# Performance work log

Hardware: AMD Instinct MI355X
Metric: run time of the kernel (lower is better)

The kernel has to match this reference:

```python
import jax, jax.numpy as jnp
import numpy as np

Z_DIM = 3
H = 128
N_BLOCKS = 4
N = 30000
E = 180000
T = 2


def _mlp2(x, W1, b1, W2, b2):
    return jnp.maximum(x @ W1 + b1, 0.0) @ W2 + b2


def _stats(x, eps=1e-8):
    # batch mean/std as accumulated by the running-stat Normalizer (buffers -> no grad)
    m = x.mean(0)
    v = jnp.maximum((x * x).mean(0) - m * m, 0.0)
    s = jnp.maximum(jnp.sqrt(v), eps)
    return jax.lax.stop_gradient(m), jax.lax.stop_gradient(s)


def setup_inputs() -> dict:
    key = jax.random.key(0)
    ks = jax.random.split(key, 32)

    def w(k, shape, fan_in):
        return jax.random.normal(k, shape, jnp.float32) / np.sqrt(fan_in).astype(np.float32)

    inp = {}
    inp["z"] = jax.random.normal(ks[0], (T, N, Z_DIM), jnp.float32)
    inp["z_target"] = jax.random.normal(ks[1], (N, Z_DIM), jnp.float32)
    inp["pos"] = jax.random.uniform(ks[2], (N, 2), jnp.float32)
    # encoder node MLP: z_dim -> H -> H
    inp["enc_node_W1"] = w(ks[3], (Z_DIM, H), Z_DIM)
    inp["enc_node_b1"] = jnp.zeros((H,), jnp.float32)
    inp["enc_node_W2"] = w(ks[4], (H, H), H)
    inp["enc_node_b2"] = jnp.zeros((H,), jnp.float32)
    # encoder edge MLP: edge_dim(3) -> H -> H
    inp["enc_edge_W1"] = w(ks[5], (3, H), 3)
    inp["enc_edge_b1"] = jnp.zeros((H,), jnp.float32)
    inp["enc_edge_W2"] = w(ks[6], (H, H), H)
    inp["enc_edge_b2"] = jnp.zeros((H,), jnp.float32)
    # decoder MLP: H -> H -> z_dim
    inp["dec_W1"] = w(ks[7], (H, H), H)
    inp["dec_b1"] = jnp.zeros((H,), jnp.float32)
    inp["dec_W2"] = w(ks[8], (H, Z_DIM), H)
    inp["dec_b2"] = jnp.zeros((Z_DIM,), jnp.float32)
    # GraphNetBlocks, stacked over n_blocks
    inp["blk_edge_W1"] = w(ks[9], (N_BLOCKS, 3 * H, H), 3 * H)
    inp["blk_edge_b1"] = jnp.zeros((N_BLOCKS, H), jnp.float32)
    inp["blk_edge_W2"] = w(ks[10], (N_BLOCKS, H, H), H)
    inp["blk_edge_b2"] = jnp.zeros((N_BLOCKS, H), jnp.float32)
    inp["blk_node_W1"] = w(ks[11], (N_BLOCKS, 2 * H, H), 2 * H)
    inp["blk_node_b1"] = jnp.zeros((N_BLOCKS, H), jnp.float32)
    inp["blk_node_W2"] = w(ks[12], (N_BLOCKS, H, H), H)
    inp["blk_node_b2"] = jnp.zeros((N_BLOCKS, H), jnp.float32)
    # bidirectional mesh edges (triangles_to_edges output)
    inp["senders"] = jax.random.randint(ks[13], (E,), 0, N, jnp.int64)
    inp["receivers"] = jax.random.randint(ks[14], (E,), 0, N, jnp.int64)
    return inp


def reference(z, z_target, pos,
              enc_node_W1, enc_node_b1, enc_node_W2, enc_node_b2,
              enc_edge_W1, enc_edge_b1, enc_edge_W2, enc_edge_b2,
              dec_W1, dec_b1, dec_W2, dec_b2,
              blk_edge_W1, blk_edge_b1, blk_edge_W2, blk_edge_b2,
              blk_node_W1, blk_node_b1, blk_node_W2, blk_node_b2,
              senders, receivers):
    zl = z[-1]                                   # [N, z_dim]
    n_nodes = zl.shape[0]

    # --- build_graph ---
    rel = pos[senders] - pos[receivers]          # [E, 2]
    ef_raw = jnp.concatenate([rel, jnp.linalg.norm(rel, axis=1, keepdims=True)], axis=1)  # [E, 3]
    em, es = _stats(ef_raw)
    ef = _mlp2((ef_raw - em) / es, enc_edge_W1, enc_edge_b1, enc_edge_W2, enc_edge_b2)    # [E, H]
    nm, ns = _stats(zl)
    nf = _mlp2((zl - nm) / ns, enc_node_W1, enc_node_b1, enc_node_W2, enc_node_b2)        # [N, H]

    # --- message passing blocks ---
    def block(carry, p):
        nf, ef = carry
        eW1, eb1, eW2, eb2, nW1, nb1, nW2, nb2 = p
        e_in = jnp.concatenate([ef, nf[senders], nf[receivers]], axis=1)   # [E, 3H]
        ef = _mlp2(e_in, eW1, eb1, eW2, eb2) + ef
        agg = jax.ops.segment_sum(ef, receivers, num_segments=n_nodes)    # [N, H]
        n_in = jnp.concatenate([nf, agg], axis=1)                          # [N, 2H]
        nf = _mlp2(n_in, nW1, nb1, nW2, nb2) + nf
        return (nf, ef), None

    (nf, ef), _ = jax.lax.scan(block, (nf, ef),
                               (blk_edge_W1, blk_edge_b1, blk_edge_W2, blk_edge_b2,
                                blk_node_W1, blk_node_b1, blk_node_W2, blk_node_b2))

    # --- decode + loss ---
    output = _mlp2(nf, dec_W1, dec_b1, dec_W2, dec_b2)                     # [N, z_dim]
    target = z_target - zl
    om, os = _stats(target)
    target_normalized = (target - om) / os
    loss = jnp.mean((target_normalized - output) ** 2)

    z_update = jax.lax.stop_gradient(output) * os + om                     # Normalizer.inverse(detach)
    z_pred = zl + z_update
    rmse = jnp.mean(jnp.sqrt(jnp.mean((z_pred - z_target) ** 2, axis=0)))
    return z_pred, loss, rmse
```

## Files before the change

### kernel.cpp

```cpp
#include <hip/hip_runtime.h>
#include <hip/hip_bf16.h>
#include <math.h>

#define HDIM 128
#define TPB 256

typedef __attribute__((ext_vector_type(8))) short bf16x8;
typedef __attribute__((ext_vector_type(4))) float f32x4;

static inline int ceil_div(int a, int b){ return (a + b - 1) / b; }

__device__ __forceinline__ float wave_sum(float v){
#pragma unroll
  for (int o = 32; o > 0; o >>= 1) v += __shfl_down(v, o, 64);
  return v;
}
__device__ __forceinline__ int wave_sum_i(int v){
#pragma unroll
  for (int o = 32; o > 0; o >>= 1) v += __shfl_down(v, o, 64);
  return v;
}

__device__ __forceinline__ short f2bf(float f){
  __hip_bfloat16 h = __float2bfloat16(f);
  return *reinterpret_cast<short*>(&h);
}
__device__ __forceinline__ float bfb2f(short s){
  unsigned int u = ((unsigned int)(unsigned short)s) << 16;
  return __builtin_bit_cast(float, u);
}

__device__ __forceinline__ void gl_lds16(const short* g, short* l){
  __builtin_amdgcn_global_load_lds(
      (const __attribute__((address_space(1))) void*)g,
      (__attribute__((address_space(3))) void*)l, 16, 0, 0);
}

__global__ void prep_a(const int* __restrict__ rcv, int* __restrict__ deg, int E, int neb,
                       const float* __restrict__ zl, const float* __restrict__ zt,
                       float* __restrict__ npart, int N, int nnb,
                       const float* __restrict__ encEW2,
                       const float* __restrict__ encNW2,
                       const float* __restrict__ decW1,
                       const float* __restrict__ beW1,
                       const float* __restrict__ beW2,
                       const float* __restrict__ bnW1,
                       const float* __restrict__ bnW2,
                       __hip_bfloat16* __restrict__ wp){
  __shared__ float red[4][12];
  const int bx = blockIdx.x, tid = threadIdx.x;
  if (bx < neb){
    int e = bx * 256 + tid;
    if (e < E) atomicAdd(&deg[rcv[e]], 1);
    return;
  }
  if (bx < neb + nnb){
    int b = bx - neb;
    int w = tid >> 6, l = tid & 63;
    int n = b * 256 + tid;
    float s[12];
#pragma unroll
    for (int i = 0; i < 12; i++) s[i] = 0.f;
    if (n < N){
#pragma unroll
      for (int d = 0; d < 3; d++){
        float z = zl[3*n+d];
        float t = zt[3*n+d] - z;
        s[d]   = z;  s[3+d] = z*z;
        s[6+d] = t;  s[9+d] = t*t;
      }
    }
#pragma unroll
    for (int i = 0; i < 12; i++) s[i] = wave_sum(s[i]);
    if (l == 0)
#pragma unroll
      for (int i = 0; i < 12; i++) red[w][i] = s[i];
    __syncthreads();
    if (tid < 12)
      npart[(size_t)b * 12 + tid] =
        red[0][tid] + red[1][tid] + red[2][tid] + red[3][tid];
    return;
  }
  int pid = bx - neb - nnb;
  int y = pid / 192;
  int x = pid - y * 192;
  const float* src; __hip_bfloat16* dst; int K;
  if (y == 0){ src = encEW2; dst = wp;          K = 128; }
  else if (y == 1){ src = encNW2; dst = wp + 16384; K = 128; }
  else if (y == 2){ src = decW1;  dst = wp + 32768; K = 128; }
  else {
    int b = (y - 3) >> 2, j = (y - 3) & 3;
    __hip_bfloat16* base = wp + 49152 + b * 114688;
    if (j == 0){ src = beW1 + b*49152; dst = base;          K = 384; }
    else if (j == 1){ src = beW2 + b*16384; dst = base + 49152; K = 128; }
    else if (j == 2){ src = bnW1 + b*32768; dst = base + 65536; K = 256; }
    else { src = bnW2 + b*16384; dst = base + 98304; K = 128; }
  }
  int id = x * 256 + tid;
  if (id >= 128 * K) return;
  int c = id >> 12;
  int r = id & 4095;
  int t = r >> 9;
  int l = (r >> 3) & 63;
  int j = r & 7;
  int k = c * 32 + ((l >> 4) << 3) + j;
  int n = t * 16 + (l & 15);
  dst[id] = __float2bfloat16(src[k * 128 + n]);
}

__global__ void scan_pass1(const int* __restrict__ deg, int* __restrict__ bsum, int N){
  __shared__ int red[4];
  int tid = threadIdx.x;
  int base = blockIdx.x * 1024;
  int s = 0;
  for (int i = tid; i < 1024; i += 256){
    int idx = base + i;
    if (idx < N) s += deg[idx];
  }
  s = wave_sum_i(s);
  if ((tid & 63) == 0) red[tid >> 6] = s;
  __syncthreads();
  if (tid == 0) bsum[blockIdx.x] = red[0] + red[1] + red[2] + red[3];
}

__global__ void scan_pass3(const int* __restrict__ deg, const int* __restrict__ bsum,
                           int nsb, int* __restrict__ row_start,
                           int* __restrict__ cursor, int N, int E){
  __shared__ int tsum[256];
  __shared__ int base_s;
  int tid = threadIdx.x;
  if (tid == 0){
    int acc = 0;
    for (int b = 0; b < (int)blockIdx.x; b++) acc += bsum[b];
    base_s = acc;
    if (blockIdx.x == 0) row_start[N] = E;
  }
  int base = blockIdx.x * 1024;
  int i0 = base + tid * 4;
  int v[4];
  int s = 0;
#pragma unroll
  for (int k = 0; k < 4; k++){
    int idx = i0 + k;
    v[k] = (idx < N) ? deg[idx] : 0;
    s += v[k];
  }
  tsum[tid] = s;
  __syncthreads();
  for (int off = 1; off < 256; off <<= 1){
    int val = (tid >= off) ? tsum[tid - off] : 0;
    __syncthreads();
    tsum[tid] += val;
    __syncthreads();
  }
  int excl = (tid == 0) ? 0 : tsum[tid - 1];
  int b = base_s + excl;
#pragma unroll
  for (int k = 0; k < 4; k++){
    int idx = i0 + k;
    if (idx < N){
      row_start[idx] = b;
      cursor[idx]    = b;
      b += v[k];
    }
  }
}

__global__ void edge_prep(const float* __restrict__ pos,
                          const int* __restrict__ snd,
                          const int* __restrict__ rcv,
                          int* __restrict__ cursor,
                          int* __restrict__ psnd,
                          int* __restrict__ prcv,
                          float* __restrict__ ef_raw,
                          float* __restrict__ epart, int E){
  __shared__ float red[4][6];
  int tid = threadIdx.x, w = tid >> 6, l = tid & 63;
  int e = blockIdx.x * blockDim.x + tid;
  float s[6] = {0.f,0.f,0.f,0.f,0.f,0.f};
  if (e < E){
    int si = snd[e], ri = rcv[e];
    int p = atomicAdd(&cursor[ri], 1);
    psnd[p] = si;
    prcv[p] = ri;
    float rx = pos[2*si]   - pos[2*ri];
    float ry = pos[2*si+1] - pos[2*ri+1];
    float nm = sqrtf(rx*rx + ry*ry);
    ef_raw[3*p]   = rx;
    ef_raw[3*p+1] = ry;
    ef_raw[3*p+2] = nm;
    s[0] = rx; s[1] = ry; s[2] = nm;
    s[3] = rx*rx; s[4] = ry*ry; s[5] = nm*nm;
  }
#pragma unroll
  for (int k = 0; k < 6; k++) s[k] = wave_sum(s[k]);
  if (l == 0)
#pragma unroll
    for (int k = 0; k < 6; k++) red[w][k] = s[k];
  __syncthreads();
  if (tid < 6)
    epart[(size_t)blockIdx.x * 6 + tid] =
      red[0][tid] + red[1][tid] + red[2][tid] + red[3][tid];
}

__global__ void reduce_finalize(const float* __restrict__ ep, int ne,
                                const float* __restrict__ np_, int nn,
                                float* __restrict__ fin, int E, int N){
  __shared__ float red[4];
  __shared__ float raw[18];
  int tid = threadIdx.x, w = tid >> 6, l = tid & 63;
  for (int j = 0; j < 6; j++){
    float s = 0.f;
    for (int b = tid; b < ne; b += 256) s += ep[(size_t)b * 6 + j];
    s = wave_sum(s);
    if (l == 0) red[w] = s;
    __syncthreads();
    if (tid == 0) raw[j] = red[0] + red[1] + red[2] + red[3];
    __syncthreads();
  }
  for (int j = 0; j < 12; j++){
    float s = 0.f;
    for (int b = tid; b < nn; b += 256) s += np_[(size_t)b * 12 + j];
    s = wave_sum(s);
    if (l == 0) red[w] = s;
    __syncthreads();
    if (tid == 0) raw[6 + j] = red[0] + red[1] + red[2] + red[3];
    __syncthreads();
  }
  if (tid == 0){
#pragma unroll
    for (int d = 0; d < 3; d++){
      float cE = (float)E, cN = (float)N;
      float m, v;
      m = raw[0+d] / cE; v = fmaxf(raw[3+d]/cE - m*m, 0.f);
      fin[0+d] = m;  fin[3+d]  = fmaxf(sqrtf(v), 1e-8f);
      m = raw[6+d] / cN; v = fmaxf(raw[9+d]/cN - m*m, 0.f);
      fin[6+d] = m;  fin[9+d]  = fmaxf(sqrtf(v), 1e-8f);
      m = raw[12+d] / cN; v = fmaxf(raw[15+d]/cN - m*m, 0.f);
      fin[12+d] = m; fin[15+d] = fmaxf(sqrtf(v), 1e-8f);
    }
  }
}

__launch_bounds__(256)
__global__ void encoder_both(const float* __restrict__ eraw,
                             const float* __restrict__ zl,
                             const float* __restrict__ fin,
                             const float* __restrict__ eW1, const float* __restrict__ eb1,
                             const float* __restrict__ nW1, const float* __restrict__ nb1,
                             const __hip_bfloat16* __restrict__ wp,
                             const float* __restrict__ eb2, const float* __restrict__ nb2,
                             __hip_bfloat16* __restrict__ efo, __hip_bfloat16* __restrict__ nfo,
                             int E, int N, int EB){
  __shared__ __align__(16) short bsh[16384];
  const int tid = threadIdx.x, w = tid >> 6, l = tid & 63, m = l & 15, q = l >> 4;
  const bool ise = ((int)blockIdx.x < EB);
  const float* raw = ise ? eraw : zl;
  const float* mptr = fin + (ise ? 0 : 6);
  const float* sptr = fin + (ise ? 3 : 9);
  const float* W1 = ise ? eW1 : nW1;
  const float* b1 = ise ? eb1 : nb1;
  const float* b2 = ise ? eb2 : nb2;
  const short* wsrc = (const short*)wp + (ise ? 0 : 16384);
  __hip_bfloat16* out = ise ? efo : nfo;
  const int rows = ise ? E : N;
  const int bx = ise ? (int)blockIdx.x : (int)blockIdx.x - EB;
#pragma unroll
  for (int i = 0; i < 8; i++){
    int inst = w * 8 + i;
    gl_lds16(wsrc + inst * 512 + l * 8, &bsh[inst * 512]);
  }
  float s0 = mptr[0], s1 = mptr[1], s2 = mptr[2];
  float d0 = sptr[0], d1 = sptr[1], d2 = sptr[2];
  const int row0 = bx * 64 + w * 16;
  const int ra = min(row0 + m, rows - 1);
  float x0 = (raw[3*ra]   - s0) / d0;
  float x1 = (raw[3*ra+1] - s1) / d1;
  float x2 = (raw[3*ra+2] - s2) / d2;
  bf16x8 afr[4];
#pragma unroll
  for (int c = 0; c < 4; c++){
    int nb = c * 32 + q * 8;
#pragma unroll
    for (int j = 0; j < 8; j++){
      float h = b1[nb+j] + x0 * W1[nb+j] + x1 * W1[128+nb+j] + x2 * W1[256+nb+j];
      afr[c][j] = f2bf(fmaxf(h, 0.f));
    }
  }
  f32x4 acc[8];
#pragma unroll
  for (int t = 0; t < 8; t++) acc[t] = (f32x4){0.f,0.f,0.f,0.f};
  __syncthreads();
#pragma unroll
  for (int c = 0; c < 4; c++){
#pragma unroll
    for (int t = 0; t < 8; t++){
      bf16x8 b = *(const bf16x8*)&bsh[(c*8 + t)*512 + l*8];
      acc[t] = __builtin_amdgcn_mfma_f32_16x16x32_bf16(afr[c], b, acc[t], 0, 0, 0);
    }
  }
  const int row_d = row0 + q * 4;
#pragma unroll
  for (int t = 0; t < 8; t++){
    int col = t * 16 + m;
    float bb = b2[col];
#pragma unroll
    for (int r = 0; r < 4; r++){
      int e = row_d + r;
      if (e < rows) out[(size_t)e * HDIM + col] = __float2bfloat16(acc[t][r] + bb);
    }
  }
}

__launch_bounds__(256)
__global__ void msg_pre(const __hip_bfloat16* __restrict__ nf,
                        const __hip_bfloat16* __restrict__ eWf,
                        __hip_bfloat16* __restrict__ u, int N){
  __shared__ __align__(16) short wsh[16384];
  const int tid = threadIdx.x, w = tid >> 6, l = tid & 63, m = l & 15, q = l >> 4;
  const short* wsrc = (const short*)eWf + 4 * 4096;
#pragma unroll
  for (int i = 0; i < 8; i++){
    int f = w * 8 + i;
    gl_lds16(wsrc + f * 512 + l * 8, &wsh[f * 512]);
  }
  const int row0 = blockIdx.x * 64 + w * 16;
  const int ra = min(row0 + m, N - 1);
  const short* pa = (const short*)nf + (size_t)ra * HDIM + q * 8;
  bf16x8 afr[4];
#pragma unroll
  for (int c = 0; c < 4; c++) afr[c] = *(const bf16x8*)(pa + c * 32);
  f32x4 acc[8];
#pragma unroll
  for (int t = 0; t < 8; t++) acc[t] = (f32x4){0.f,0.f,0.f,0.f};
  __syncthreads();
#pragma unroll
  for (int c = 0; c < 4; c++)
#pragma unroll
    for (int t = 0; t < 8; t++){
      bf16x8 b = *(const bf16x8*)&wsh[(c*8 + t)*512 + l*8];
      acc[t] = __builtin_amdgcn_mfma_f32_16x16x32_bf16(afr[c], b, acc[t], 0, 0, 0);
    }
  const int row_d = row0 + q * 4;
#pragma unroll
  for (int t = 0; t < 8; t++){
    int col = t * 16 + m;
#pragma unroll
    for (int r = 0; r < 4; r++){
      int n = row_d + r;
      if (n < N) u[(size_t)n * 256 + col] = __float2bfloat16(acc[t][r]);
    }
  }
  __syncthreads();
#pragma unroll
  for (int i = 0; i < 8; i++){
    int f = w * 8 + i;
    gl_lds16(wsrc + 16384 + f * 512 + l * 8, &wsh[f * 512]);
  }
#pragma unroll
  for (int t = 0; t < 8; t++) acc[t] = (f32x4){0.f,0.f,0.f,0.f};
  __syncthreads();
#pragma unroll
  for (int c = 0; c < 4; c++)
#pragma unroll
    for (int t = 0; t < 8; t++){
      bf16x8 b = *(const bf16x8*)&wsh[(c*8 + t)*512 + l*8];
      acc[t] = __builtin_amdgcn_mfma_f32_16x16x32_bf16(afr[c], b, acc[t], 0, 0, 0);
    }
#pragma unroll
  for (int t = 0; t < 8; t++){
    int col = 128 + t * 16 + m;
#pragma unroll
    for (int r = 0; r < 4; r++){
      int n = row_d + r;
      if (n < N) u[(size_t)n * 256 + col] = __float2bfloat16(acc[t][r]);
    }
  }
}

__launch_bounds__(512, 6)
__global__ void edge_block(const int* __restrict__ psnd,
                           const int* __restrict__ prcv,
                           const __hip_bfloat16* __restrict__ u,
                           __hip_bfloat16* __restrict__ ef,
                           const __hip_bfloat16* __restrict__ Wfrag,
                           const float* __restrict__ b1,
                           const float* __restrict__ b2,
                           int E){
  __shared__ __align__(16) short bsh[8192];
  __shared__ __align__(16) short hsh[8][16][136];
  const int tid = threadIdx.x, w = tid >> 6, l = tid & 63, m = l & 15, q = l >> 4;
  const short* wsrc = (const short*)Wfrag;
  const int row0 = blockIdx.x * 128 + w * 16;
  const int grow = min(row0 + (l >> 2), E - 1);
  const int us_row = psnd[grow], ur_row = prcv[grow];
  gl_lds16(wsrc + (w*2)  *512 + l*8, &bsh[(w*2)  *512]);
  gl_lds16(wsrc + (w*2+1)*512 + l*8, &bsh[(w*2+1)*512]);
  const int ra = min(row0 + m, E - 1);
  const short* pe = (const short*)ef + (size_t)ra * HDIM + q * 8;
  bf16x8 afr[4];
#pragma unroll
  for (int c = 0; c < 4; c++) afr[c] = *(const bf16x8*)(pe + c * 32);
  {
    const short* pus = (const short*)u + (size_t)us_row * 256 + (l & 3) * 32;
    const short* pur = (const short*)u + (size_t)ur_row * 256 + 128 + (l & 3) * 32;
    short* hdst = &hsh[w][l >> 2][(l & 3) * 32];
#pragma unroll
    for (int k = 0; k < 4; k++){
      bf16x8 a = *(const bf16x8*)(pus + k * 8);
      bf16x8 b = *(const bf16x8*)(pur + k * 8);
      bf16x8 s;
#pragma unroll
      for (int j = 0; j < 8; j++) s[j] = f2bf(bfb2f(a[j]) + bfb2f(b[j]));
      *(bf16x8*)(hdst + k * 8) = s;
    }
  }
  f32x4 acc[8];
#pragma unroll
  for (int t = 0; t < 8; t++) acc[t] = (f32x4){0.f,0.f,0.f,0.f};
  __syncthreads();
#pragma unroll
  for (int cc = 0; cc < 2; cc++)
#pragma unroll
    for (int t = 0; t < 8; t++){
      bf16x8 b = *(const bf16x8*)&bsh[(cc*8 + t)*512 + l*8];
      acc[t] = __builtin_amdgcn_mfma_f32_16x16x32_bf16(afr[cc], b, acc[t], 0, 0, 0);
    }
  __syncthreads();
  gl_lds16(wsrc + 8192 + (w*2)  *512 + l*8, &bsh[(w*2)  *512]);
  gl_lds16(wsrc + 8192 + (w*2+1)*512 + l*8, &bsh[(w*2+1)*512]);
  __syncthreads();
#pragma unroll
  for (int cc = 0; cc < 2; cc++)
#pragma unroll
    for (int t = 0; t < 8; t++){
      bf16x8 b = *(const bf16x8*)&bsh[(cc*8 + t)*512 + l*8];
      acc[t] = __builtin_amdgcn_mfma_f32_16x16x32_bf16(afr[2+cc], b, acc[t], 0, 0, 0);
    }
  __syncthreads();
  gl_lds16(wsrc + 49152 + (w*2)  *512 + l*8, &bsh[(w*2)  *512]);
  gl_lds16(wsrc + 49152 + (w*2+1)*512 + l*8, &bsh[(w*2+1)*512]);
#pragma unroll
  for (int t = 0; t < 8; t++){
    float bb = b1[t * 16 + m];
#pragma unroll
    for (int r = 0; r < 4; r++){
      float uval = bfb2f(hsh[w][q*4 + r][t*16 + m]);
      hsh[w][q*4 + r][t*16 + m] = f2bf(fmaxf(acc[t][r] + uval + bb, 0.f));
    }
  }
  __syncthreads();
  bf16x8 ah[4];
  const short* ph = &hsh[w][m][0] + q * 8;
#pragma unroll
  for (int c = 0; c < 4; c++) ah[c] = *(const bf16x8*)(ph + c * 32);
#pragma unroll
  for (int t = 0; t < 8; t++) acc[t] = (f32x4){0.f,0.f,0.f,0.f};
#pragma unroll
  for (int cc = 0; cc < 2; cc++)
#pragma unroll
    for (int t = 0; t < 8; t++){
      bf16x8 b = *(const bf16x8*)&bsh[(cc*8 + t)*512 + l*8];
      acc[t] = __builtin_amdgcn_mfma_f32_16x16x32_bf16(ah[cc], b, acc[t], 0, 0, 0);
    }
  __syncthreads();
  gl_lds16(wsrc + 57344 + (w*2)  *512 + l*8, &bsh[(w*2)  *512]);
  gl_lds16(wsrc + 57344 + (w*2+1)*512 + l*8, &bsh[(w*2+1)*512]);
  const int orow = row0 + (l >> 2);
  const int orc = min(orow, E - 1);
  const short* pold = (const short*)ef + (size_t)orc * HDIM + (l & 3) * 32;
  bf16x8 vold[4];
#pragma unroll
  for (int k = 0; k < 4; k++) vold[k] = *(const bf16x8*)(pold + k * 8);
  __syncthreads();
#pragma unroll
  for (int cc = 0; cc < 2; cc++)
#pragma unroll
    for (int t = 0; t < 8; t++){
      bf16x8 b = *(const bf16x8*)&bsh[(cc*8 + t)*512 + l*8];
      acc[t] = __builtin_amdgcn_mfma_f32_16x16x32_bf16(ah[2+cc], b, acc[t], 0, 0, 0);
    }
#pragma unroll
  for (int t = 0; t < 8; t++){
    float bb = b2[t * 16 + m];
#pragma unroll
    for (int r = 0; r < 4; r++)
      hsh[w][q*4 + r][t*16 + m] = f2bf(acc[t][r] + bb);
  }
  if (orow < E){
    const short* src = &hsh[w][l >> 2][(l & 3) * 32];
    short* dst = (short*)ef + (size_t)orow * HDIM + (l & 3) * 32;
#pragma unroll
    for (int k = 0; k < 4; k++){
      bf16x8 vnew = *(const bf16x8*)(src + k * 8);
      bf16x8 vr;
#pragma unroll
      for (int j = 0; j < 8; j++) vr[j] = f2bf(bfb2f(vnew[j]) + bfb2f(vold[k][j]));
      *(bf16x8*)(dst + k * 8) = vr;
    }
  }
}

#define NB_COMPUTE_CHUNK(c) do {                                               \
  const short* bb_ = &bsh[(((c) >> 1) & 1) * 8192 + ((c) & 1) * 4096];         \
  _Pragma("unroll")                                                            \
  for (int t = 0; t < 8; t++){                                                 \
    bf16x8 b = *(const bf16x8*)(bb_ + t * 512 + l * 8);                        \
    acc[t] = __builtin_amdgcn_mfma_f32_16x16x32_bf16(afr[c], b, acc[t], 0, 0, 0); \
  }                                                                            \
} while(0)

__launch_bounds__(256)
__global__ void node_block(const int* __restrict__ row_start,
                           const __hip_bfloat16* __restrict__ ef,
                           __hip_bfloat16* __restrict__ nf,
                           const __hip_bfloat16* __restrict__ Wfrag,
                           const float* __restrict__ b1,
                           const float* __restrict__ b2,
                           int N){
  __shared__ __align__(16) short bsh[16384];
  __shared__ __align__(16) short hsh[4][16][136];
  const int tid = threadIdx.x, w = tid >> 6, l = tid & 63, m = l & 15, q = l >> 4;
  const short* wsrc = (const short*)Wfrag;
  auto stage_pair = [&](int p){
    const short* s = wsrc + p * 8192;
    short* d = &bsh[(p & 1) * 8192];
#pragma unroll
    for (int i = 0; i < 4; i++)
      gl_lds16(s + (i*4 + w)*512 + l*8, d + (i*4 + w)*512);
  };
  stage_pair(0); stage_pair(1);

  const int row0 = blockIdx.x * 64 + w * 16;
  const int ra = min(row0 + m, N - 1);
  const short* pn = (const short*)nf + (size_t)ra * HDIM + q * 8;
  bf16x8 afr[8];
#pragma unroll
  for (int c = 0; c < 4; c++) afr[c] = *(const bf16x8*)(pn + c * 32);

  float sum[4][8];
#pragma unroll
  for (int c = 0; c < 4; c++)
#pragma unroll
    for (int j = 0; j < 8; j++) sum[c][j] = 0.f;
  int s0 = row_start[ra], s1 = row_start[ra + 1];
  for (int it = s0; it < s1; it++){
    const short* pf = (const short*)ef + (size_t)it * HDIM + q * 8;
#pragma unroll
    for (int c = 0; c < 4; c++){
      bf16x8 v = *(const bf16x8*)(pf + c * 32);
#pragma unroll
      for (int j = 0; j < 8; j++) sum[c][j] += bfb2f(v[j]);
    }
  }
#pragma unroll
  for (int c = 0; c < 4; c++)
#pragma unroll
    for (int j = 0; j < 8; j++) afr[4 + c][j] = f2bf(sum[c][j]);

  f32x4 acc[8];
#pragma unroll
  for (int t = 0; t < 8; t++) acc[t] = (f32x4){0.f,0.f,0.f,0.f};
  __syncthreads();
  NB_COMPUTE_CHUNK(0);
  NB_COMPUTE_CHUNK(1);
  __syncthreads();
  stage_pair(2);
  NB_COMPUTE_CHUNK(2);
  NB_COMPUTE_CHUNK(3);
  __syncthreads();
  stage_pair(3);
  NB_COMPUTE_CHUNK(4);
  NB_COMPUTE_CHUNK(5);
  __syncthreads();
  NB_COMPUTE_CHUNK(6);
  NB_COMPUTE_CHUNK(7);
  __syncthreads();
  {
    const short* s = wsrc + 32768;
#pragma unroll
    for (int i = 0; i < 8; i++)
      gl_lds16(s + (i*4 + w)*512 + l*8, &bsh[(i*4 + w)*512]);
  }
#pragma unroll
  for (int t = 0; t < 8; t++){
    float bb = b1[t * 16 + m];
#pragma unroll
    for (int r = 0; r < 4; r++)
      hsh[w][q*4 + r][t*16 + m] = f2bf(fmaxf(acc[t][r] + bb, 0.f));
  }
  __syncthreads();
  const short* ph = &hsh[w][m][0] + q * 8;
#pragma unroll
  for (int t = 0; t < 8; t++) acc[t] = (f32x4){0.f,0.f,0.f,0.f};
#pragma unroll
  for (int c = 0; c < 4; c++){
    bf16x8 a = *(const bf16x8*)(ph + c * 32);
#pragma unroll
    for (int t = 0; t < 8; t++){
      bf16x8 b = *(const bf16x8*)&bsh[(c*8 + t)*512 + l*8];
      acc[t] = __builtin_amdgcn_mfma_f32_16x16x32_bf16(a, b, acc[t], 0, 0, 0);
    }
  }
#pragma unroll
  for (int t = 0; t < 8; t++){
    float bb = b2[t * 16 + m];
#pragma unroll
    for (int r = 0; r < 4; r++)
      hsh[w][q*4 + r][t*16 + m] = f2bf(acc[t][r] + bb);
  }
  const int orow = row0 + (l >> 2);
  if (orow < N){
    const short* pold = (const short*)nf + (size_t)orow * HDIM + (l & 3) * 32;
    const short* src = &hsh[w][l >> 2][(l & 3) * 32];
    short* dst = (short*)nf + (size_t)orow * HDIM + (l & 3) * 32;
#pragma unroll
    for (int k = 0; k < 4; k++){
      bf16x8 vnew = *(const bf16x8*)(src + k * 8);
      bf16x8 vo   = *(const bf16x8*)(pold + k * 8);
      bf16x8 vr;
#pragma unroll
      for (int j = 0; j < 8; j++) vr[j] = f2bf(bfb2f(vnew[j]) + bfb2f(vo[j]));
      *(bf16x8*)(dst + k * 8) = vr;
    }
  }
}

__launch_bounds__(256)
__global__ void dec_fused(const __hip_bfloat16* __restrict__ A,
                          const __hip_bfloat16* __restrict__ Wf,
                          const float* __restrict__ b1,
                          const float* __restrict__ W2,
                          const float* __restrict__ b2,
                          const float* __restrict__ zl,
                          const float* __restrict__ z_target,
                          const float* __restrict__ fin,
                          float* __restrict__ d_out,
                          float* __restrict__ lred,
                          unsigned int* __restrict__ cnt,
                          int N){
  __shared__ __align__(16) short bsh[16384];
  __shared__ float Wl[HDIM * 3];
  __shared__ float red[4][4];
  const int tid = threadIdx.x, w = tid >> 6, l = tid & 63, m = l & 15, q = l >> 4;
  const short* wsrc = (const short*)Wf;
#pragma unroll
  for (int i = 0; i < 8; i++){
    int inst = w * 8 + i;
    gl_lds16(wsrc + inst * 512 + l * 8, &bsh[inst * 512]);
  }
  for (int i = tid; i < HDIM * 3; i += 256) Wl[i] = W2[i];
  const int row0 = blockIdx.x * 64 + w * 16;
  const int ra = min(row0 + m, N - 1);
  const short* pa = (const short*)A + (size_t)ra * HDIM + q * 8;
  bf16x8 afr[4];
#pragma unroll
  for (int c = 0; c < 4; c++) afr[c] = *(const bf16x8*)(pa + c * 32);
  f32x4 acc[8];
#pragma unroll
  for (int t = 0; t < 8; t++) acc[t] = (f32x4){0.f,0.f,0.f,0.f};
  __syncthreads();
#pragma unroll
  for (int c = 0; c < 4; c++){
#pragma unroll
    for (int t = 0; t < 8; t++){
      bf16x8 b = *(const bf16x8*)&bsh[(c*8 + t)*512 + l*8];
      acc[t] = __builtin_amdgcn_mfma_f32_16x16x32_bf16(afr[c], b, acc[t], 0, 0, 0);
    }
  }
  float p0[4] = {0,0,0,0}, p1[4] = {0,0,0,0}, p2[4] = {0,0,0,0};
#pragma unroll
  for (int t = 0; t < 8; t++){
    int col = t * 16 + m;
    float bb = b1[col];
    float w0 = Wl[col*3], w1 = Wl[col*3+1], w2 = Wl[col*3+2];
#pragma unroll
    for (int r = 0; r < 4; r++){
      float h = fmaxf(acc[t][r] + bb, 0.f);
      p0[r] += h * w0; p1[r] += h * w1; p2[r] += h * w2;
    }
  }
#pragma unroll
  for (int r = 0; r < 4; r++){
#pragma unroll
    for (int o = 1; o < 16; o <<= 1){
      p0[r] += __shfl_xor(p0[r], o, 64);
      p1[r] += __shfl_xor(p1[r], o, 64);
      p2[r] += __shfl_xor(p2[r], o, 64);
    }
  }
  float s[4] = {0.f,0.f,0.f,0.f};
  if (m == 0){
#pragma unroll
    for (int r = 0; r < 4; r++){
      int n = row0 + q * 4 + r;
      if (n < N){
        float pd[3] = {p0[r], p1[r], p2[r]};
#pragma unroll
        for (int d = 0; d < 3; d++){
          float o   = pd[d] + b2[d];
          float om = fin[12 + d], os = fin[15 + d];
          float zld = zl[3*n + d];
          float zt  = z_target[3*n + d];
          float tn  = ((zt - zld) - om) / os;
          float diff = tn - o;
          s[0] += diff * diff;
          float zp = zld + o * os + om;
          d_out[3*n + d] = zp;
          float e = zp - zt;
          s[1 + d] += e * e;
        }
      }
    }
  }
#pragma unroll
  for (int k = 0; k < 4; k++) s[k] = wave_sum(s[k]);
  if (l == 0)
#pragma unroll
    for (int k = 0; k < 4; k++) red[w][k] = s[k];
  __syncthreads();
  if (tid < 4)
    atomicAdd(&lred[tid], red[0][tid] + red[1][tid] + red[2][tid] + red[3][tid]);
  __syncthreads();
  if (tid == 0){
    __threadfence();
    unsigned int t = atomicAdd(cnt, 1u);
    if (t == gridDim.x - 1){
      float vals[4];
#pragma unroll
      for (int k = 0; k < 4; k++) vals[k] = atomicAdd(&lred[k], 0.f);
      float cN = (float)N;
      float loss = vals[0] / (3.f * cN);
      float rmse = (sqrtf(vals[1]/cN) + sqrtf(vals[2]/cN) + sqrtf(vals[3]/cN)) / 3.f;
      d_out[(size_t)3 * N]     = loss;
      d_out[(size_t)3 * N + 1] = rmse;
    }
  }
}

extern "C" void kernel_launch(void* const* d_in, const int* in_sizes, int n_in,
                              void* d_out, int out_size, void* d_ws, size_t ws_size,
                              hipStream_t stream){
  const float* z           = (const float*)d_in[0];
  const float* z_target    = (const float*)d_in[1];
  const float* pos         = (const float*)d_in[2];
  const float* enc_node_W1 = (const float*)d_in[3];
  const float* enc_node_b1 = (const float*)d_in[4];
  const float* enc_node_W2 = (const float*)d_in[5];
  const float* enc_node_b2 = (const float*)d_in[6];
  const float* enc_edge_W1 = (const float*)d_in[7];
  const float* enc_edge_b1 = (const float*)d_in[8];
  const float* enc_edge_W2 = (const float*)d_in[9];
  const float* enc_edge_b2 = (const float*)d_in[10];
  const float* dec_W1      = (const float*)d_in[11];
  const float* dec_b1      = (const float*)d_in[12];
  const float* dec_W2      = (const float*)d_in[13];
  const float* dec_b2      = (const float*)d_in[14];
  const float* blk_edge_W1 = (const float*)d_in[15];
  const float* blk_edge_b1 = (const float*)d_in[16];
  const float* blk_edge_W2 = (const float*)d_in[17];
  const float* blk_edge_b2 = (const float*)d_in[18];
  const float* blk_node_W1 = (const float*)d_in[19];
  const float* blk_node_b1 = (const float*)d_in[20];
  const float* blk_node_W2 = (const float*)d_in[21];
  const float* blk_node_b2 = (const float*)d_in[22];
  const int*   senders     = (const int*)d_in[23];
  const int*   receivers   = (const int*)d_in[24];

  const int N = in_sizes[1] / 3;
  const int E = in_sizes[23];
  const float* zl = z + (size_t)N * 3;

  const int neb = ceil_div(E, TPB);
  const int nnb = ceil_div(N, TPB);
  const int nsb = ceil_div(N, 1024);
  const int EB  = ceil_div(E, 64);
  const int NB  = ceil_div(N, 64);

  char* p = (char*)d_ws;
  auto carve = [&](size_t bytes) -> char* {
    char* r = p; p += (bytes + 255) & ~(size_t)255; return r;
  };
  float* stats_fin = (float*)carve(32 * 4);
  float* epart     = (float*)carve((size_t)neb * 6 * 4);
  float* npart     = (float*)carve((size_t)nnb * 12 * 4);
  float* ef_raw    = (float*)carve((size_t)E * 3 * 4);
  int*   deg       = (int*)carve((size_t)(N + 16) * 4);
  float* lred      = (float*)(deg + N);
  unsigned int* cnt = (unsigned int*)(deg + N + 4);
  int*   bsum      = (int*)carve((size_t)(nsb + 1) * 4);
  int*   row_start = (int*)carve((size_t)(N + 1) * 4);
  int*   cursor    = (int*)carve((size_t)N * 4);
  int*   psnd      = (int*)carve((size_t)E * 4);
  int*   prcv      = (int*)carve((size_t)E * 4);
  __hip_bfloat16* wp = (__hip_bfloat16*)carve((size_t)507904 * 2);
  __hip_bfloat16* ef = (__hip_bfloat16*)carve((size_t)E * HDIM * 2);
  __hip_bfloat16* nf = (__hip_bfloat16*)carve((size_t)N * HDIM * 2);
  __hip_bfloat16* u  = (__hip_bfloat16*)carve((size_t)N * 256 * 2);

  float* out = (float*)d_out;

  hipMemsetAsync(deg, 0, (size_t)(N + 16) * 4, stream);

  prep_a<<<neb + nnb + 3648, TPB, 0, stream>>>(receivers, deg, E, neb,
                                               zl, z_target, npart, N, nnb,
                                               enc_edge_W2, enc_node_W2, dec_W1,
                                               blk_edge_W1, blk_edge_W2,
                                               blk_node_W1, blk_node_W2, wp);
  scan_pass1<<<nsb, TPB, 0, stream>>>(deg, bsum, N);
  scan_pass3<<<nsb, TPB, 0, stream>>>(deg, bsum, nsb, row_start, cursor, N, E);
  edge_prep<<<neb, TPB, 0, stream>>>(pos, senders, receivers, cursor,
                                     psnd, prcv, ef_raw, epart, E);
  reduce_finalize<<<1, TPB, 0, stream>>>(epart, neb, npart, nnb, stats_fin, E, N);

  encoder_both<<<EB + NB, TPB, 0, stream>>>(ef_raw, zl, stats_fin,
                                            enc_edge_W1, enc_edge_b1,
                                            enc_node_W1, enc_node_b1,
                                            wp, enc_edge_b2, enc_node_b2,
                                            ef, nf, E, N, EB);

  for (int b = 0; b < 4; b++){
    const __hip_bfloat16* eWf = wp + 49152 + (size_t)b * 114688;
    const __hip_bfloat16* nWf = eWf + 65536;
    const float* eb1 = blk_edge_b1 + (size_t)b * 128;
    const float* eb2 = blk_edge_b2 + (size_t)b * 128;
    const float* nb1 = blk_node_b1 + (size_t)b * 128;
    const float* nb2 = blk_node_b2 + (size_t)b * 128;

    msg_pre<<<NB, TPB, 0, stream>>>(nf, eWf, u, N);
    edge_block<<<ceil_div(E, 128), 512, 0, stream>>>(psnd, prcv, u, ef,
                                                     eWf, eb1, eb2, E);
    node_block<<<NB, TPB, 0, stream>>>(row_start, ef, nf,
                                       nWf, nb1, nb2, N);
  }

  dec_fused<<<NB, TPB, 0, stream>>>(nf, wp + 32768, dec_b1, dec_W2, dec_b2,
                                    zl, z_target, stats_fin,
                                    out, lred, cnt, N);
}
```

Before: 522.6 us.

## Fuse edge-to-node aggregation into edge kernel via run-length atomic adds

```diff
diff --git a/kernel.cpp b/kernel.cpp
--- a/kernel.cpp
+++ b/kernel.cpp
@@ -124,8 +124,7 @@
 }
 
 __global__ void scan_pass3(const int* __restrict__ deg, const int* __restrict__ bsum,
-                           int nsb, int* __restrict__ row_start,
-                           int* __restrict__ cursor, int N, int E){
+                           int nsb, int* __restrict__ cursor, int N){
   __shared__ int tsum[256];
   __shared__ int base_s;
   int tid = threadIdx.x;
@@ -133,7 +132,6 @@
     int acc = 0;
     for (int b = 0; b < (int)blockIdx.x; b++) acc += bsum[b];
     base_s = acc;
-    if (blockIdx.x == 0) row_start[N] = E;
   }
   int base = blockIdx.x * 1024;
   int i0 = base + tid * 4;
@@ -159,8 +157,7 @@
   for (int k = 0; k < 4; k++){
     int idx = i0 + k;
     if (idx < N){
-      row_start[idx] = b;
-      cursor[idx]    = b;
+      cursor[idx] = b;
       b += v[k];
     }
   }
@@ -315,7 +312,8 @@
 __launch_bounds__(256)
 __global__ void msg_pre(const __hip_bfloat16* __restrict__ nf,
                         const __hip_bfloat16* __restrict__ eWf,
-                        __hip_bfloat16* __restrict__ u, int N){
+                        __hip_bfloat16* __restrict__ u,
+                        float* __restrict__ agg, int N){
   __shared__ __align__(16) short wsh[16384];
   const int tid = threadIdx.x, w = tid >> 6, l = tid & 63, m = l & 15, q = l >> 4;
   const short* wsrc = (const short*)eWf + 4 * 4096;
@@ -323,6 +321,12 @@
   for (int i = 0; i < 8; i++){
     int f = w * 8 + i;
     gl_lds16(wsrc + f * 512 + l * 8, &wsh[f * 512]);
+  }
+  {
+    float* az = agg + (size_t)blockIdx.x * 8192;
+#pragma unroll
+    for (int i = 0; i < 8; i++)
+      *(f32x4*)(az + (size_t)(i * 256 + tid) * 4) = (f32x4){0.f,0.f,0.f,0.f};
   }
   const int row0 = blockIdx.x * 64 + w * 16;
   const int ra = min(row0 + m, N - 1);
@@ -378,7 +382,7 @@
   }
 }
 
-__launch_bounds__(512, 6)
+__launch_bounds__(512)
 __global__ void edge_block(const int* __restrict__ psnd,
                            const int* __restrict__ prcv,
                            const __hip_bfloat16* __restrict__ u,
@@ -386,16 +390,22 @@
                            const __hip_bfloat16* __restrict__ Wfrag,
                            const float* __restrict__ b1,
                            const float* __restrict__ b2,
-                           int E){
-  __shared__ __align__(16) short bsh[8192];
+                           float* __restrict__ agg,
+                           int do_write, int E){
+  __shared__ __align__(16) short bsh[16384];
   __shared__ __align__(16) short hsh[8][16][136];
+  __shared__ int rsh[8][16];
   const int tid = threadIdx.x, w = tid >> 6, l = tid & 63, m = l & 15, q = l >> 4;
   const short* wsrc = (const short*)Wfrag;
   const int row0 = blockIdx.x * 128 + w * 16;
   const int grow = min(row0 + (l >> 2), E - 1);
   const int us_row = psnd[grow], ur_row = prcv[grow];
-  gl_lds16(wsrc + (w*2)  *512 + l*8, &bsh[(w*2)  *512]);
-  gl_lds16(wsrc + (w*2+1)*512 + l*8, &bsh[(w*2+1)*512]);
+  if ((l & 3) == 0) rsh[w][l >> 2] = ur_row;
+#pragma unroll
+  for (int i = 0; i < 4; i++){
+    int inst = i * 8 + w;
+    gl_lds16(wsrc + inst * 512 + l * 8, &bsh[inst * 512]);
+  }
   const int ra = min(row0 + m, E - 1);
   const short* pe = (const short*)ef + (size_t)ra * HDIM + q * 8;
   bf16x8 afr[4];
@@ -420,26 +430,19 @@
   for (int t = 0; t < 8; t++) acc[t] = (f32x4){0.f,0.f,0.f,0.f};
   __syncthreads();
 #pragma unroll
-  for (int cc = 0; cc < 2; cc++)
+  for (int c = 0; c < 4; c++){
 #pragma unroll
     for (int t = 0; t < 8; t++){
-      bf16x8 b = *(const bf16x8*)&bsh[(cc*8 + t)*512 + l*8];
-      acc[t] = __builtin_amdgcn_mfma_f32_16x16x32_bf16(afr[cc], b, acc[t], 0, 0, 0);
-    }
-  __syncthreads();
-  gl_lds16(wsrc + 8192 + (w*2)  *512 + l*8, &bsh[(w*2)  *512]);
-  gl_lds16(wsrc + 8192 + (w*2+1)*512 + l*8, &bsh[(w*2+1)*512]);
-  __syncthreads();
-#pragma unroll
-  for (int cc = 0; cc < 2; cc++)
-#pragma unroll
-    for (int t = 0; t < 8; t++){
-      bf16x8 b = *(const bf16x8*)&bsh[(cc*8 + t)*512 + l*8];
-      acc[t] = __builtin_amdgcn_mfma_f32_16x16x32_bf16(afr[2+cc], b, acc[t], 0, 0, 0);
-    }
-  __syncthreads();
-  gl_lds16(wsrc + 49152 + (w*2)  *512 + l*8, &bsh[(w*2)  *512]);
-  gl_lds16(wsrc + 49152 + (w*2+1)*512 + l*8, &bsh[(w*2+1)*512]);
+      bf16x8 b = *(const bf16x8*)&bsh[(c*8 + t)*512 + l*8];
+      acc[t] = __builtin_amdgcn_mfma_f32_16x16x32_bf16(afr[c], b, acc[t], 0, 0, 0);
+    }
+  }
+  __syncthreads();
+#pragma unroll
+  for (int i = 0; i < 4; i++){
+    int inst = i * 8 + w;
+    gl_lds16(wsrc + 49152 + inst * 512 + l * 8, &bsh[inst * 512]);
+  }
 #pragma unroll
   for (int t = 0; t < 8; t++){
     float bb = b1[t * 16 + m];
@@ -457,46 +460,57 @@
 #pragma unroll
   for (int t = 0; t < 8; t++) acc[t] = (f32x4){0.f,0.f,0.f,0.f};
 #pragma unroll
-  for (int cc = 0; cc < 2; cc++)
+  for (int c = 0; c < 4; c++){
 #pragma unroll
     for (int t = 0; t < 8; t++){
-      bf16x8 b = *(const bf16x8*)&bsh[(cc*8 + t)*512 + l*8];
-      acc[t] = __builtin_amdgcn_mfma_f32_16x16x32_bf16(ah[cc], b, acc[t], 0, 0, 0);
-    }
-  __syncthreads();
-  gl_lds16(wsrc + 57344 + (w*2)  *512 + l*8, &bsh[(w*2)  *512]);
-  gl_lds16(wsrc + 57344 + (w*2+1)*512 + l*8, &bsh[(w*2+1)*512]);
+      bf16x8 b = *(const bf16x8*)&bsh[(c*8 + t)*512 + l*8];
+      acc[t] = __builtin_amdgcn_mfma_f32_16x16x32_bf16(ah[c], b, acc[t], 0, 0, 0);
+    }
+  }
+#pragma unroll
+  for (int t = 0; t < 8; t++){
+    float bb = b2[t * 16 + m];
+#pragma unroll
+    for (int r = 0; r < 4; r++)
+      hsh[w][q*4 + r][t*16 + m] = f2bf(acc[t][r] + bb);
+  }
   const int orow = row0 + (l >> 2);
   const int orc = min(orow, E - 1);
   const short* pold = (const short*)ef + (size_t)orc * HDIM + (l & 3) * 32;
-  bf16x8 vold[4];
-#pragma unroll
-  for (int k = 0; k < 4; k++) vold[k] = *(const bf16x8*)(pold + k * 8);
-  __syncthreads();
-#pragma unroll
-  for (int cc = 0; cc < 2; cc++)
-#pragma unroll
-    for (int t = 0; t < 8; t++){
-      bf16x8 b = *(const bf16x8*)&bsh[(cc*8 + t)*512 + l*8];
-      acc[t] = __builtin_amdgcn_mfma_f32_16x16x32_bf16(ah[2+cc], b, acc[t], 0, 0, 0);
-    }
-#pragma unroll
-  for (int t = 0; t < 8; t++){
-    float bb = b2[t * 16 + m];
-#pragma unroll
-    for (int r = 0; r < 4; r++)
-      hsh[w][q*4 + r][t*16 + m] = f2bf(acc[t][r] + bb);
-  }
-  if (orow < E){
-    const short* src = &hsh[w][l >> 2][(l & 3) * 32];
-    short* dst = (short*)ef + (size_t)orow * HDIM + (l & 3) * 32;
-#pragma unroll
-    for (int k = 0; k < 4; k++){
-      bf16x8 vnew = *(const bf16x8*)(src + k * 8);
-      bf16x8 vr;
-#pragma unroll
-      for (int j = 0; j < 8; j++) vr[j] = f2bf(bfb2f(vnew[j]) + bfb2f(vold[k][j]));
-      *(bf16x8*)(dst + k * 8) = vr;
+  short* hslot = &hsh[w][l >> 2][(l & 3) * 32];
+  short* dst = (short*)ef + (size_t)orc * HDIM + (l & 3) * 32;
+  const bool wr = (orow < E) && do_write;
+#pragma unroll
+  for (int k = 0; k < 4; k++){
+    bf16x8 vnew = *(const bf16x8*)(hslot + k * 8);
+    bf16x8 vo   = *(const bf16x8*)(pold + k * 8);
+    bf16x8 vr;
+#pragma unroll
+    for (int j = 0; j < 8; j++) vr[j] = f2bf(bfb2f(vnew[j]) + bfb2f(vo[j]));
+    *(bf16x8*)(hslot + k * 8) = vr;
+    if (wr) *(bf16x8*)(dst + k * 8) = vr;
+  }
+  {
+    const int c0 = l * 2, c1 = l * 2 + 1;
+    float run0 = 0.f, run1 = 0.f;
+    int cur = -1;
+#pragma unroll 1
+    for (int e = 0; e < 16; e++){
+      if (row0 + e >= E) break;
+      int rv = rsh[w][e];
+      if (rv != cur){
+        if (cur >= 0){
+          atomicAdd(&agg[(size_t)cur * 128 + c0], run0);
+          atomicAdd(&agg[(size_t)cur * 128 + c1], run1);
+        }
+        cur = rv; run0 = 0.f; run1 = 0.f;
+      }
+      run0 += bfb2f(hsh[w][e][c0]);
+      run1 += bfb2f(hsh[w][e][c1]);
+    }
+    if (cur >= 0){
+      atomicAdd(&agg[(size_t)cur * 128 + c0], run0);
+      atomicAdd(&agg[(size_t)cur * 128 + c1], run1);
     }
   }
 }
@@ -511,8 +525,7 @@
 } while(0)
 
 __launch_bounds__(256)
-__global__ void node_block(const int* __restrict__ row_start,
-                           const __hip_bfloat16* __restrict__ ef,
+__global__ void node_block(const float* __restrict__ agg,
                            __hip_bfloat16* __restrict__ nf,
                            const __hip_bfloat16* __restrict__ Wfrag,
                            const float* __restrict__ b1,
@@ -538,25 +551,17 @@
 #pragma unroll
   for (int c = 0; c < 4; c++) afr[c] = *(const bf16x8*)(pn + c * 32);
 
-  float sum[4][8];
-#pragma unroll
-  for (int c = 0; c < 4; c++)
-#pragma unroll
-    for (int j = 0; j < 8; j++) sum[c][j] = 0.f;
-  int s0 = row_start[ra], s1 = row_start[ra + 1];
-  for (int it = s0; it < s1; it++){
-    const short* pf = (const short*)ef + (size_t)it * HDIM + q * 8;
-#pragma unroll
-    for (int c = 0; c < 4; c++){
-      bf16x8 v = *(const bf16x8*)(pf + c * 32);
-#pragma unroll
-      for (int j = 0; j < 8; j++) sum[c][j] += bfb2f(v[j]);
-    }
-  }
-#pragma unroll
-  for (int c = 0; c < 4; c++)
-#pragma unroll
-    for (int j = 0; j < 8; j++) afr[4 + c][j] = f2bf(sum[c][j]);
+  const float* pag = agg + (size_t)ra * 128 + q * 8;
+#pragma unroll
+  for (int c = 0; c < 4; c++){
+    f32x4 a0 = *(const f32x4*)(pag + c * 32);
+    f32x4 a1 = *(const f32x4*)(pag + c * 32 + 4);
+#pragma unroll
+    for (int j = 0; j < 4; j++){
+      afr[4 + c][j]     = f2bf(a0[j]);
+      afr[4 + c][4 + j] = f2bf(a1[j]);
+    }
+  }
 
   f32x4 acc[8];
 #pragma unroll
@@ -789,10 +794,10 @@
   float* lred      = (float*)(deg + N);
   unsigned int* cnt = (unsigned int*)(deg + N + 4);
   int*   bsum      = (int*)carve((size_t)(nsb + 1) * 4);
-  int*   row_start = (int*)carve((size_t)(N + 1) * 4);
   int*   cursor    = (int*)carve((size_t)N * 4);
   int*   psnd      = (int*)carve((size_t)E * 4);
   int*   prcv      = (int*)carve((size_t)E * 4);
+  float* agg       = (float*)carve(((size_t)N + 64) * 128 * 4);
   __hip_bfloat16* wp = (__hip_bfloat16*)carve((size_t)507904 * 2);
   __hip_bfloat16* ef = (__hip_bfloat16*)carve((size_t)E * HDIM * 2);
   __hip_bfloat16* nf = (__hip_bfloat16*)carve((size_t)N * HDIM * 2);
@@ -808,7 +813,7 @@
                                                blk_edge_W1, blk_edge_W2,
                                                blk_node_W1, blk_node_W2, wp);
   scan_pass1<<<nsb, TPB, 0, stream>>>(deg, bsum, N);
-  scan_pass3<<<nsb, TPB, 0, stream>>>(deg, bsum, nsb, row_start, cursor, N, E);
+  scan_pass3<<<nsb, TPB, 0, stream>>>(deg, bsum, nsb, cursor, N);
   edge_prep<<<neb, TPB, 0, stream>>>(pos, senders, receivers, cursor,
                                      psnd, prcv, ef_raw, epart, E);
   reduce_finalize<<<1, TPB, 0, stream>>>(epart, neb, npart, nnb, stats_fin, E, N);
@@ -827,11 +832,11 @@
     const float* nb1 = blk_node_b1 + (size_t)b * 128;
     const float* nb2 = blk_node_b2 + (size_t)b * 128;
 
-    msg_pre<<<NB, TPB, 0, stream>>>(nf, eWf, u, N);
+    msg_pre<<<NB, TPB, 0, stream>>>(nf, eWf, u, agg, N);
     edge_block<<<ceil_div(E, 128), 512, 0, stream>>>(psnd, prcv, u, ef,
-                                                     eWf, eb1, eb2, E);
-    node_block<<<NB, TPB, 0, stream>>>(row_start, ef, nf,
-                                       nWf, nb1, nb2, N);
+                                                     eWf, eb1, eb2, agg,
+                                                     (b < 3) ? 1 : 0, E);
+    node_block<<<NB, TPB, 0, stream>>>(agg, nf, nWf, nb1, nb2, N);
   }
 
   dec_fused<<<NB, TPB, 0, stream>>>(nf, wp + 32768, dec_b1, dec_W2, dec_b2,
```

New measurement: 522.7 us. Within noise of the previous version (+0.0%).
